# Optimization experiments

Measured on AMD Instinct MI355X. Metric: run time of the kernel, lower is better.

The kernel has to match this reference:

```python
import jax, jax.numpy as jnp
import numpy as np
from jax.ops import segment_sum, segment_max

N = 50000          # nodes
E = 1_600_000      # edges (before self-loops)
IN = 16            # in_channels
F = 20             # N_features
H1 = 4             # heads in conv1
EDGE_DIM = 7
OUT = 3            # out_channels
NEG_SLOPE = 0.2


def setup_inputs() -> dict:
    key = jax.random.key(0)
    ks = jax.random.split(key, 24)
    g = lambda k, shape, fan: (jax.random.normal(k, shape, jnp.float32)
                               * (1.0 / np.sqrt(fan)))
    inp = {}
    inp["x"] = jax.random.normal(ks[0], (N, IN), jnp.float32)
    inp["edge_index"] = jax.random.randint(ks[1], (2, E), 0, N, jnp.int32)
    inp["edge_attr"] = jax.random.normal(ks[2], (E, EDGE_DIM), jnp.float32)
    # conv1: IN -> F, heads=H1, edge_dim=EDGE_DIM
    inp["W1"] = g(ks[3], (IN, H1 * F), IN)
    inp["att_src1"] = g(ks[4], (H1, F), F)
    inp["att_dst1"] = g(ks[5], (H1, F), F)
    inp["We1"] = g(ks[6], (EDGE_DIM, H1 * F), EDGE_DIM)
    inp["att_e1"] = g(ks[7], (H1, F), F)
    inp["b1"] = jnp.zeros((H1 * F,), jnp.float32)
    # conv2: (H1*F) -> F, heads=1, edge_dim=EDGE_DIM
    inp["W2"] = g(ks[8], (H1 * F, F), H1 * F)
    inp["att_src2"] = g(ks[9], (1, F), F)
    inp["att_dst2"] = g(ks[10], (1, F), F)
    inp["We2"] = g(ks[11], (EDGE_DIM, F), EDGE_DIM)
    inp["att_e2"] = g(ks[12], (1, F), F)
    inp["b2"] = jnp.zeros((F,), jnp.float32)
    # decoder: F -> 10 -> OUT
    inp["D1w"] = g(ks[13], (F, 10), F)
    inp["D1b"] = jnp.zeros((10,), jnp.float32)
    inp["D2w"] = g(ks[14], (10, OUT), 10)
    inp["D2b"] = jnp.zeros((OUT,), jnp.float32)
    return inp


def _gat_layer(x, src, dst, eattr, W, a_s, a_d, We, a_e, b, heads, fdim):
    """PyG GATConv (shared src/dst lin, add_self_loops already applied)."""
    n = x.shape[0]
    xh = (x @ W).reshape(n, heads, fdim)                  # [N,H,F]
    eh = (eattr @ We).reshape(-1, heads, fdim)            # [Ea,H,F]
    a_src = jnp.sum(xh * a_s, axis=-1)                    # [N,H]
    a_dst = jnp.sum(xh * a_d, axis=-1)                    # [N,H]
    a_edge = jnp.sum(eh * a_e, axis=-1)                   # [Ea,H]
    logits = a_src[src] + a_dst[dst] + a_edge             # [Ea,H]
    logits = jnp.where(logits >= 0, logits, NEG_SLOPE * logits)
    # segment softmax over destination node
    m = segment_max(logits, dst, num_segments=n)          # [N,H]
    ex = jnp.exp(logits - m[dst])
    denom = segment_sum(ex, dst, num_segments=n)          # [N,H]
    alpha = ex / (denom[dst] + 1e-16)                     # [Ea,H]
    msg = xh[src] * alpha[:, :, None]                     # [Ea,H,F]
    out = segment_sum(msg, dst, num_segments=n)           # [N,H,F]
    return out.reshape(n, heads * fdim) + b


def reference(x, edge_index, edge_attr, W1, att_src1, att_dst1, We1, att_e1,
              b1, W2, att_src2, att_dst2, We2, att_e2, b2, D1w, D1b, D2w, D2b):
    src, dst = edge_index[0], edge_index[1]
    # add self-loops with edge_attr fill_value='mean' (scatter-mean by dst)
    deg = segment_sum(jnp.ones((E,), jnp.float32), dst, num_segments=N)
    mean_attr = segment_sum(edge_attr, dst, num_segments=N) \
        / jnp.maximum(deg, 1.0)[:, None]
    loops = jnp.arange(N, dtype=src.dtype)
    src_a = jnp.concatenate([src, loops])
    dst_a = jnp.concatenate([dst, loops])
    eattr_a = jnp.concatenate([edge_attr, mean_attr], axis=0)
    # conv1 (heads=4, concat) -> elu  (dropouts are no-ops in eval)
    h = _gat_layer(x, src_a, dst_a, eattr_a, W1, att_src1, att_dst1,
                   We1, att_e1, b1, H1, F)
    h = jax.nn.elu(h)
    # conv2 (heads=1) -> elu
    h = _gat_layer(h, src_a, dst_a, eattr_a, W2, att_src2, att_dst2,
                   We2, att_e2, b2, 1, F)
    h = jax.nn.elu(h)
    # decoder MLP
    h = jax.nn.relu(h @ D1w + D1b)
    return h @ D2w + D2b
```

## Files before the change

kernel.cpp:

```cpp
#include <hip/hip_runtime.h>
#include <hip/hip_fp16.h>

constexpr int NN  = 50000;
constexpr int EEg = 1600000;
constexpr int IND = 16;
constexpr int FD  = 20;
constexpr int H1D = 4;
constexpr int ED  = 7;
constexpr int OUTD = 3;
constexpr int FP  = 24;

__device__ __forceinline__ float lrelu(float x) { return x >= 0.0f ? x : 0.2f * x; }
__device__ __forceinline__ float elu(float x)   { return x > 0.0f ? x : expm1f(x); }
__device__ __forceinline__ unsigned pack2(float a, float b) {
    __half2 h = __floats2half2_rn(a, b);
    return *(unsigned*)&h;
}
__device__ __forceinline__ float2 up2(unsigned w) {
    __half2 h = *(__half2*)&w;
    return __half22float2(h);
}

__global__ void k_deg(const int* __restrict__ ei, int* __restrict__ deg,
                      int* __restrict__ rank) {
    int e = blockIdx.x * blockDim.x + threadIdx.x;
    if (e >= EEg) return;
    rank[e] = atomicAdd(&deg[ei[EEg + e]], 1);
}

__global__ void k_ve(const float* __restrict__ We1, const float* __restrict__ ae1,
                     const float* __restrict__ We2, const float* __restrict__ ae2,
                     float* __restrict__ ve1, float* __restrict__ ve2) {
    int t = threadIdx.x;
    if (t < ED * H1D) {
        int d = t >> 2, h = t & 3;
        float s = 0.0f;
        for (int f = 0; f < FD; ++f) s += We1[d * (H1D * FD) + h * FD + f] * ae1[h * FD + f];
        ve1[t] = s;
    } else if (t < ED * H1D + ED) {
        int d = t - ED * H1D;
        float s = 0.0f;
        for (int f = 0; f < FD; ++f) s += We2[d * FD + f] * ae2[f];
        ve2[d] = s;
    }
}

__global__ void k_scanA(const int* __restrict__ deg, int* __restrict__ partial,
                        int* __restrict__ bsum) {
    __shared__ int sd[256];
    int t = threadIdx.x, i = blockIdx.x * 256 + t;
    int v = (i < NN) ? deg[i] : 0;
    sd[t] = v;
    __syncthreads();
    for (int off = 1; off < 256; off <<= 1) {
        int u = (t >= off) ? sd[t - off] : 0;
        __syncthreads();
        sd[t] += u;
        __syncthreads();
    }
    if (i < NN) partial[i] = sd[t] - v;
    if (t == 255) bsum[blockIdx.x] = sd[255];
}
__global__ void k_scanB(const int* __restrict__ bsum, int* __restrict__ boff, int nb) {
    __shared__ int sd[256];
    int t = threadIdx.x;
    int v = (t < nb) ? bsum[t] : 0;
    sd[t] = v;
    __syncthreads();
    for (int off = 1; off < 256; off <<= 1) {
        int u = (t >= off) ? sd[t - off] : 0;
        __syncthreads();
        sd[t] += u;
        __syncthreads();
    }
    if (t < nb) boff[t] = sd[t] - v;
}
__global__ void k_scanC(const int* __restrict__ partial, const int* __restrict__ boff,
                        int* __restrict__ row_off) {
    int i = blockIdx.x * 256 + threadIdx.x;
    if (i < NN) row_off[i] = partial[i] + boff[blockIdx.x];
    if (i == 0) row_off[NN] = EEg;
}

__global__ __launch_bounds__(256) void k_scatter(
        const int* __restrict__ ei, const float* __restrict__ eattr,
        const float* __restrict__ ve1, const float* __restrict__ ve2,
        const int* __restrict__ row_off, const int* __restrict__ rank,
        uint4* __restrict__ csr) {
    __shared__ float sv1[ED * H1D], sv2[ED];
    __shared__ float se[256 * ED];
    if (threadIdx.x < ED * H1D) sv1[threadIdx.x] = ve1[threadIdx.x];
    if (threadIdx.x < ED) sv2[threadIdx.x] = ve2[threadIdx.x];
    size_t gbase = (size_t)blockIdx.x * 256 * ED;
    for (int i = threadIdx.x; i < 256 * ED; i += 256) {
        size_t g = gbase + i;
        if (g < (size_t)EEg * ED) se[i] = eattr[g];
    }
    __syncthreads();
    int e = blockIdx.x * 256 + threadIdx.x;
    if (e >= EEg) return;
    int src = ei[e], dst = ei[EEg + e];
    const float* a = &se[threadIdx.x * ED];
    float v0 = 0.f, v1 = 0.f, v2 = 0.f, v3 = 0.f, w2 = 0.f;
#pragma unroll
    for (int d = 0; d < ED; ++d) {
        float ad = a[d];
        v0 += ad * sv1[d * H1D + 0];
        v1 += ad * sv1[d * H1D + 1];
        v2 += ad * sv1[d * H1D + 2];
        v3 += ad * sv1[d * H1D + 3];
        w2 += ad * sv2[d];
    }
    int slot = row_off[dst] + rank[e];
    uint4 rec;
    rec.x = (unsigned)src;
    rec.y = pack2(v0, v1);
    rec.z = pack2(v2, v3);
    rec.w = pack2(w2, 0.0f);
    csr[slot] = rec;
}

__global__ void k_mean_self(const int* __restrict__ row_off, const uint4* __restrict__ csr,
                            float* __restrict__ a_e1s, float* __restrict__ a_e2s) {
    int n = blockIdx.x * blockDim.x + threadIdx.x;
    if (n >= NN) return;
    int beg = row_off[n], end = row_off[n + 1];
    float s0 = 0.f, s1 = 0.f, s2 = 0.f, s3 = 0.f, se = 0.f;
    for (int j = beg; j < end; ++j) {
        uint4 r = csr[j];
        float2 a01 = up2(r.y), a23 = up2(r.z), ap = up2(r.w);
        s0 += a01.x; s1 += a01.y; s2 += a23.x; s3 += a23.y; se += ap.x;
    }
    float inv = 1.0f / fmaxf((float)(end - beg), 1.0f);
    a_e1s[n * H1D + 0] = s0 * inv;
    a_e1s[n * H1D + 1] = s1 * inv;
    a_e1s[n * H1D + 2] = s2 * inv;
    a_e1s[n * H1D + 3] = s3 * inv;
    a_e2s[n] = se * inv;
}

__global__ void k_xh1attn1(const float* __restrict__ x, const float* __restrict__ W1,
                           const float* __restrict__ as, const float* __restrict__ ad,
                           __half* __restrict__ xh1h, float* __restrict__ a_src1,
                           float* __restrict__ a_dst1) {
    __shared__ float sW[IND * H1D * FD];
    for (int i = threadIdx.x; i < IND * H1D * FD; i += blockDim.x) sW[i] = W1[i];
    __syncthreads();
    int idx = blockIdx.x * blockDim.x + threadIdx.x;
    if (idx >= NN * H1D) return;
    int n = idx >> 2, h = idx & 3;
    float xr[IND];
    const float4* xp = (const float4*)&x[(size_t)n * IND];
#pragma unroll
    for (int q = 0; q < IND / 4; ++q) {
        float4 v = xp[q];
        xr[4 * q] = v.x; xr[4 * q + 1] = v.y; xr[4 * q + 2] = v.z; xr[4 * q + 3] = v.w;
    }
    float ss = 0.f, sd = 0.f;
    float o[FD];
#pragma unroll
    for (int f = 0; f < FD; ++f) {
        float s = 0.f;
#pragma unroll
        for (int k = 0; k < IND; ++k) s += xr[k] * sW[k * (H1D * FD) + h * FD + f];
        o[f] = s;
        ss += s * as[h * FD + f];
        sd += s * ad[h * FD + f];
    }
    uint4* xo = (uint4*)&xh1h[((size_t)n * H1D + h) * FP];
    xo[0] = make_uint4(pack2(o[0], o[1]), pack2(o[2], o[3]), pack2(o[4], o[5]), pack2(o[6], o[7]));
    xo[1] = make_uint4(pack2(o[8], o[9]), pack2(o[10], o[11]), pack2(o[12], o[13]), pack2(o[14], o[15]));
    xo[2] = make_uint4(pack2(o[16], o[17]), pack2(o[18], o[19]), 0u, 0u);
    a_src1[idx] = ss; a_dst1[idx] = sd;
}

#define FMA_PAYLOAD(ex, g0, g1, g2)                                     \
    {                                                                   \
        float2 f_;                                                      \
        f_ = up2(g0.x); acc[0] += (ex) * f_.x;  acc[1] += (ex) * f_.y;  \
        f_ = up2(g0.y); acc[2] += (ex) * f_.x;  acc[3] += (ex) * f_.y;  \
        f_ = up2(g0.z); acc[4] += (ex) * f_.x;  acc[5] += (ex) * f_.y;  \
        f_ = up2(g0.w); acc[6] += (ex) * f_.x;  acc[7] += (ex) * f_.y;  \
        f_ = up2(g1.x); acc[8] += (ex) * f_.x;  acc[9] += (ex) * f_.y;  \
        f_ = up2(g1.y); acc[10] += (ex) * f_.x; acc[11] += (ex) * f_.y; \
        f_ = up2(g1.z); acc[12] += (ex) * f_.x; acc[13] += (ex) * f_.y; \
        f_ = up2(g1.w); acc[14] += (ex) * f_.x; acc[15] += (ex) * f_.y; \
        f_ = up2(g2.x); acc[16] += (ex) * f_.x; acc[17] += (ex) * f_.y; \
        f_ = up2(g2.y); acc[18] += (ex) * f_.x; acc[19] += (ex) * f_.y; \
    }

__global__ __launch_bounds__(256) void k_conv1(
        const int* __restrict__ row_off, const uint4* __restrict__ csr,
        const float* __restrict__ a_src1, const float* __restrict__ a_dst1,
        const float* __restrict__ a_e1s, const __half* __restrict__ xh1h,
        const float* __restrict__ b1, float* __restrict__ h1) {
    int idx = blockIdx.x * 256 + threadIdx.x;
    int n = idx >> 4, low = idx & 15, h = low & 3, p = low >> 2;
    int beg = row_off[n], end = row_off[n + 1];
    float adst = a_dst1[n * H1D + h];
    float m, denom;
    float acc[FD];
#pragma unroll
    for (int f = 0; f < FD; ++f) acc[f] = 0.f;
    if (p == 0) {
        m = lrelu(a_src1[n * H1D + h] + adst + a_e1s[n * H1D + h]);
        denom = 1.0f;
        const uint4* xp = (const uint4*)&xh1h[((size_t)n * H1D + h) * FP];
        uint4 s0 = xp[0], s1 = xp[1];
        uint2 s2 = *(const uint2*)(xp + 2);
        FMA_PAYLOAD(1.0f, s0, s1, s2);
    } else {
        m = -1e30f; denom = 0.f;
    }
    int j = beg + p;
    uint4 rC, gC0, gC1; uint2 gC2; float avC;
    uint4 rN;
    if (j < end) {
        rC = csr[j];
        int s = (int)rC.x;
        avC = a_src1[s * H1D + h];
        const uint4* xp = (const uint4*)&xh1h[((size_t)s * H1D + h) * FP];
        gC0 = xp[0]; gC1 = xp[1]; gC2 = *(const uint2*)(xp + 2);
    }
    if (j + 4 < end) rN = csr[j + 4];
    while (j < end) {
        uint4 rNN;
        if (j + 8 < end) rNN = csr[j + 8];
        float avP; uint4 gP0, gP1; uint2 gP2;
        if (j + 4 < end) {
            int s = (int)rN.x;
            avP = a_src1[s * H1D + h];
            const uint4* xp = (const uint4*)&xh1h[((size_t)s * H1D + h) * FP];
            gP0 = xp[0]; gP1 = xp[1]; gP2 = *(const uint2*)(xp + 2);
        }
        unsigned wae = (h < 2) ? rC.y : rC.z;
        float2 aep = up2(wae);
        float ae = (h & 1) ? aep.y : aep.x;
        float l = lrelu(avC + adst + ae);
        if (l > m) {
            float sc = __expf(m - l);
            denom *= sc;
#pragma unroll
            for (int f = 0; f < FD; ++f) acc[f] *= sc;
            m = l;
        }
        float ex = __expf(l - m);
        denom += ex;
        FMA_PAYLOAD(ex, gC0, gC1, gC2);
        rC = rN; avC = avP; gC0 = gP0; gC1 = gP1; gC2 = gP2;
        rN = rNN;
        j += 4;
    }
#pragma unroll
    for (int st = 4; st <= 8; st <<= 1) {
        float mo = __shfl_xor(m, st);
        float dno = __shfl_xor(denom, st);
        float M = fmaxf(m, mo);
        float ssf = __expf(m - M), sof = __expf(mo - M);
        denom = denom * ssf + dno * sof;
#pragma unroll
        for (int f = 0; f < FD; ++f) acc[f] = acc[f] * ssf + __shfl_xor(acc[f], st) * sof;
        m = M;
    }
    if (p) return;
    float inv = 1.0f / (denom + 1e-16f);
    float* ho = &h1[((size_t)n * H1D + h) * FD];
#pragma unroll
    for (int f = 0; f < FD; ++f) ho[f] = elu(acc[f] * inv + b1[h * FD + f]);
}

__global__ void k_xh2attn2(const float* __restrict__ h1, const float* __restrict__ W2,
                           const float* __restrict__ as, const float* __restrict__ ad,
                           __half* __restrict__ xh2h, float* __restrict__ a_src2,
                           float* __restrict__ a_dst2) {
    __shared__ float sW[H1D * FD * FD];
    for (int i = threadIdx.x; i < H1D * FD * FD; i += blockDim.x) sW[i] = W2[i];
    __syncthreads();
    int n = blockIdx.x * blockDim.x + threadIdx.x;
    if (n >= NN) return;
    float hr[H1D * FD];
    const float4* hp = (const float4*)&h1[(size_t)n * (H1D * FD)];
#pragma unroll
    for (int q = 0; q < (H1D * FD) / 4; ++q) {
        float4 v = hp[q];
        hr[4 * q] = v.x; hr[4 * q + 1] = v.y; hr[4 * q + 2] = v.z; hr[4 * q + 3] = v.w;
    }
    float ss = 0.f, sd = 0.f;
    float o[FD];
#pragma unroll
    for (int f = 0; f < FD; ++f) {
        float s = 0.f;
#pragma unroll
        for (int k = 0; k < H1D * FD; ++k) s += hr[k] * sW[k * FD + f];
        o[f] = s;
        ss += s * as[f];
        sd += s * ad[f];
    }
    uint4* xo = (uint4*)&xh2h[(size_t)n * FP];
    xo[0] = make_uint4(pack2(o[0], o[1]), pack2(o[2], o[3]), pack2(o[4], o[5]), pack2(o[6], o[7]));
    xo[1] = make_uint4(pack2(o[8], o[9]), pack2(o[10], o[11]), pack2(o[12], o[13]), pack2(o[14], o[15]));
    xo[2] = make_uint4(pack2(o[16], o[17]), pack2(o[18], o[19]), 0u, 0u);
    a_src2[n] = ss; a_dst2[n] = sd;
}

__global__ __launch_bounds__(256) void k_conv2dec(
        const int* __restrict__ row_off, const uint4* __restrict__ csr,
        const float* __restrict__ a_src2, const float* __restrict__ a_dst2,
        const float* __restrict__ a_e2s, const __half* __restrict__ xh2h,
        const float* __restrict__ b2, const float* __restrict__ D1w,
        const float* __restrict__ D1b, const float* __restrict__ D2w,
        const float* __restrict__ D2b, float* __restrict__ out) {
    __shared__ float sD1w[FD * 10], sD1b[10], sD2w[10 * OUTD], sD2b[OUTD], sb2[FD];
    for (int i = threadIdx.x; i < FD * 10; i += blockDim.x) sD1w[i] = D1w[i];
    if (threadIdx.x < 10) sD1b[threadIdx.x] = D1b[threadIdx.x];
    if (threadIdx.x < 10 * OUTD) sD2w[threadIdx.x] = D2w[threadIdx.x];
    if (threadIdx.x < OUTD) sD2b[threadIdx.x] = D2b[threadIdx.x];
    if (threadIdx.x < FD) sb2[threadIdx.x] = b2[threadIdx.x];
    __syncthreads();
    int idx = blockIdx.x * 256 + threadIdx.x;
    if (idx >= NN * 4) return;
    int n = idx >> 2, p = idx & 3;
    int beg = row_off[n], end = row_off[n + 1];
    float adst = a_dst2[n];
    float m, denom;
    float acc[FD];
#pragma unroll
    for (int f = 0; f < FD; ++f) acc[f] = 0.f;
    if (p == 0) {
        m = lrelu(a_src2[n] + adst + a_e2s[n]);
        denom = 1.0f;
        const uint4* xp = (const uint4*)&xh2h[(size_t)n * FP];
        uint4 s0 = xp[0], s1 = xp[1];
        uint2 s2 = *(const uint2*)(xp + 2);
        FMA_PAYLOAD(1.0f, s0, s1, s2);
    } else {
        m = -1e30f; denom = 0.f;
    }
    int j = beg + p;
    uint4 rC, gC0, gC1; uint2 gC2; float avC;
    uint4 rN;
    if (j < end) {
        rC = csr[j];
        int s = (int)rC.x;
        avC = a_src2[s];
        const uint4* xp = (const uint4*)&xh2h[(size_t)s * FP];
        gC0 = xp[0]; gC1 = xp[1]; gC2 = *(const uint2*)(xp + 2);
    }
    if (j + 4 < end) rN = csr[j + 4];
    while (j < end) {
        uint4 rNN;
        if (j + 8 < end) rNN = csr[j + 8];
        float avP; uint4 gP0, gP1; uint2 gP2;
        if (j + 4 < end) {
            int s = (int)rN.x;
            avP = a_src2[s];
            const uint4* xp = (const uint4*)&xh2h[(size_t)s * FP];
            gP0 = xp[0]; gP1 = xp[1]; gP2 = *(const uint2*)(xp + 2);
        }
        float l = lrelu(avC + adst + up2(rC.w).x);
        if (l > m) {
            float sc = __expf(m - l);
            denom *= sc;
#pragma unroll
            for (int f = 0; f < FD; ++f) acc[f] *= sc;
            m = l;
        }
        float ex = __expf(l - m);
        denom += ex;
        FMA_PAYLOAD(ex, gC0, gC1, gC2);
        rC = rN; avC = avP; gC0 = gP0; gC1 = gP1; gC2 = gP2;
        rN = rNN;
        j += 4;
    }
#pragma unroll
    for (int st = 1; st <= 2; st <<= 1) {
        float mo = __shfl_xor(m, st);
        float dno = __shfl_xor(denom, st);
        float M = fmaxf(m, mo);
        float ssf = __expf(m - M), sof = __expf(mo - M);
        denom = denom * ssf + dno * sof;
#pragma unroll
        for (int f = 0; f < FD; ++f) acc[f] = acc[f] * ssf + __shfl_xor(acc[f], st) * sof;
        m = M;
    }
    if (p) return;
    float inv = 1.0f / (denom + 1e-16f);
    float h2[FD];
#pragma unroll
    for (int f = 0; f < FD; ++f) h2[f] = elu(acc[f] * inv + sb2[f]);
    float o[OUTD];
#pragma unroll
    for (int k = 0; k < OUTD; ++k) o[k] = sD2b[k];
    for (int j2 = 0; j2 < 10; ++j2) {
        float hid = sD1b[j2];
#pragma unroll
        for (int f = 0; f < FD; ++f) hid += h2[f] * sD1w[f * 10 + j2];
        hid = fmaxf(hid, 0.0f);
#pragma unroll
        for (int k = 0; k < OUTD; ++k) o[k] += hid * sD2w[j2 * OUTD + k];
    }
#pragma unroll
    for (int k = 0; k < OUTD; ++k) out[n * OUTD + k] = o[k];
}

extern "C" void kernel_launch(void* const* d_in, const int* in_sizes, int n_in,
                              void* d_out, int out_size, void* d_ws, size_t ws_size,
                              hipStream_t stream) {
    const float* x     = (const float*)d_in[0];
    const int*   ei    = (const int*)d_in[1];
    const float* eattr = (const float*)d_in[2];
    const float* W1    = (const float*)d_in[3];
    const float* as1   = (const float*)d_in[4];
    const float* ad1   = (const float*)d_in[5];
    const float* We1   = (const float*)d_in[6];
    const float* ae1   = (const float*)d_in[7];
    const float* b1    = (const float*)d_in[8];
    const float* W2    = (const float*)d_in[9];
    const float* as2   = (const float*)d_in[10];
    const float* ad2   = (const float*)d_in[11];
    const float* We2   = (const float*)d_in[12];
    const float* ae2   = (const float*)d_in[13];
    const float* b2    = (const float*)d_in[14];
    const float* D1w   = (const float*)d_in[15];
    const float* D1b   = (const float*)d_in[16];
    const float* D2w   = (const float*)d_in[17];
    const float* D2b   = (const float*)d_in[18];
    float* out = (float*)d_out;

    float* w = (float*)d_ws;
    size_t o = 0;
    int*   deg = (int*)(w + o); o += NN;
    size_t zero_bytes = o * sizeof(float);
    int*   rank    = (int*)(w + o); o += EEg;
    int*   partial = (int*)(w + o); o += NN;
    int*   bsum    = (int*)(w + o); o += 256;
    int*   boff    = (int*)(w + o); o += 256;
    int*   row_off = (int*)(w + o); o += NN + 4;
    float* csr     = w + o; o += (size_t)EEg * 4;
    float* ve1     = w + o; o += 32;
    float* ve2     = w + o; o += 8;
    float* a_e1s   = w + o; o += (size_t)NN * H1D;
    float* a_e2s   = w + o; o += NN;
    float* a_src1  = w + o; o += (size_t)NN * H1D;
    float* a_dst1  = w + o; o += (size_t)NN * H1D;
    __half* xh1h   = (__half*)(w + o); o += (size_t)NN * H1D * FP / 2;
    float* h1      = w + o; o += (size_t)NN * H1D * FD;
    __half* xh2h   = (__half*)(w + o); o += (size_t)NN * FP / 2;
    float* a_src2  = w + o; o += NN;
    float* a_dst2  = w + o; o += NN;

    hipMemsetAsync(d_ws, 0, zero_bytes, stream);

    const int B = 256;
    auto cdiv = [](long a, long b) { return (int)((a + b - 1) / b); };
    const int NB = cdiv(NN, 256);

    k_deg<<<cdiv(EEg, B), B, 0, stream>>>(ei, deg, rank);
    k_ve<<<1, 64, 0, stream>>>(We1, ae1, We2, ae2, ve1, ve2);
    k_scanA<<<NB, 256, 0, stream>>>(deg, partial, bsum);
    k_scanB<<<1, 256, 0, stream>>>(bsum, boff, NB);
    k_scanC<<<NB, 256, 0, stream>>>(partial, boff, row_off);
    k_scatter<<<cdiv(EEg, B), B, 0, stream>>>(ei, eattr, ve1, ve2, row_off, rank,
                                              (uint4*)csr);
    k_mean_self<<<NB, 256, 0, stream>>>(row_off, (const uint4*)csr, a_e1s, a_e2s);
    k_xh1attn1<<<cdiv((long)NN * H1D, B), B, 0, stream>>>(x, W1, as1, ad1, xh1h, a_src1,
                                                          a_dst1);
    k_conv1<<<cdiv((long)NN * 16, 256), 256, 0, stream>>>(row_off, (const uint4*)csr,
                                                          a_src1, a_dst1, a_e1s, xh1h, b1,
                                                          h1);
    k_xh2attn2<<<NB, 256, 0, stream>>>(h1, W2, as2, ad2, xh2h, a_src2, a_dst2);
    k_conv2dec<<<cdiv((long)NN * 4, 256), 256, 0, stream>>>(row_off, (const uint4*)csr,
                                                            a_src2, a_dst2, a_e2s, xh2h,
                                                            b2, D1w, D1b, D2w, D2b, out);
}
```

Baseline: 280.2 us.

## Replace atomic-rank CSR build with two-pass LSD radix bucketing by destination

Builds the destination-sorted edge list with a two-pass radix partition instead of a global atomic degree count plus scan. The first pass histograms the low 8 bits of dst per block and scatters packed records to a temporary buffer using shared-memory atomics. The second pass buckets each bin by the high bits to produce the final CSR with per-node begin and degree arrays. This removes the contended global atomics, the rank array and the memset. In exchange it adds an extra full pass over the edge records, packs dst into the upper 16 bits of a record word (which fits only because N is at most 65535), and the first kernel launches only 256 blocks.

```diff
diff --git a/kernel.cpp b/kernel.cpp
--- a/kernel.cpp
+++ b/kernel.cpp
@@ -9,6 +9,9 @@
 constexpr int ED  = 7;
 constexpr int OUTD = 3;
 constexpr int FP  = 24;
+constexpr int NB2 = 256;
+constexpr int EPB = EEg / NB2;
+constexpr int NH  = 196;
 
 __device__ __forceinline__ float lrelu(float x) { return x >= 0.0f ? x : 0.2f * x; }
 __device__ __forceinline__ float elu(float x)   { return x > 0.0f ? x : expm1f(x); }
@@ -19,13 +22,6 @@
 __device__ __forceinline__ float2 up2(unsigned w) {
     __half2 h = *(__half2*)&w;
     return __half22float2(h);
-}
-
-__global__ void k_deg(const int* __restrict__ ei, int* __restrict__ deg,
-                      int* __restrict__ rank) {
-    int e = blockIdx.x * blockDim.x + threadIdx.x;
-    if (e >= EEg) return;
-    rank[e] = atomicAdd(&deg[ei[EEg + e]], 1);
 }
 
 __global__ void k_ve(const float* __restrict__ We1, const float* __restrict__ ae1,
@@ -45,86 +41,132 @@
     }
 }
 
-__global__ void k_scanA(const int* __restrict__ deg, int* __restrict__ partial,
-                        int* __restrict__ bsum) {
+__global__ __launch_bounds__(256) void k_h1(const int* __restrict__ ei,
+                                            int* __restrict__ bh1T) {
+    __shared__ int lh[256];
+    lh[threadIdx.x] = 0;
+    __syncthreads();
+    int base0 = blockIdx.x * EPB;
+    for (int off = 0; off < EPB; off += 256) {
+        int i = off + threadIdx.x;
+        if (i < EPB) atomicAdd(&lh[ei[EEg + base0 + i] & 255], 1);
+    }
+    __syncthreads();
+    bh1T[threadIdx.x * NB2 + blockIdx.x] = lh[threadIdx.x];
+}
+
+__global__ void k_colscan(const int* __restrict__ bh1T, int* __restrict__ off1,
+                          int* __restrict__ binStart) {
+    int tid = threadIdx.x;
+    int total = 0;
+#pragma unroll 8
+    for (int b = 0; b < NB2; ++b) total += bh1T[tid * NB2 + b];
     __shared__ int sd[256];
-    int t = threadIdx.x, i = blockIdx.x * 256 + t;
-    int v = (i < NN) ? deg[i] : 0;
-    sd[t] = v;
+    sd[tid] = total;
     __syncthreads();
     for (int off = 1; off < 256; off <<= 1) {
-        int u = (t >= off) ? sd[t - off] : 0;
+        int u = (tid >= off) ? sd[tid - off] : 0;
         __syncthreads();
-        sd[t] += u;
+        sd[tid] += u;
         __syncthreads();
     }
-    if (i < NN) partial[i] = sd[t] - v;
-    if (t == 255) bsum[blockIdx.x] = sd[255];
-}
-__global__ void k_scanB(const int* __restrict__ bsum, int* __restrict__ boff, int nb) {
-    __shared__ int sd[256];
-    int t = threadIdx.x;
-    int v = (t < nb) ? bsum[t] : 0;
-    sd[t] = v;
-    __syncthreads();
-    for (int off = 1; off < 256; off <<= 1) {
-        int u = (t >= off) ? sd[t - off] : 0;
-        __syncthreads();
-        sd[t] += u;
-        __syncthreads();
-    }
-    if (t < nb) boff[t] = sd[t] - v;
-}
-__global__ void k_scanC(const int* __restrict__ partial, const int* __restrict__ boff,
-                        int* __restrict__ row_off) {
-    int i = blockIdx.x * 256 + threadIdx.x;
-    if (i < NN) row_off[i] = partial[i] + boff[blockIdx.x];
-    if (i == 0) row_off[NN] = EEg;
-}
-
-__global__ __launch_bounds__(256) void k_scatter(
+    int excl = sd[tid] - total;
+    binStart[tid] = excl;
+    if (tid == 255) binStart[256] = excl + total;
+    int run = excl;
+#pragma unroll 8
+    for (int b = 0; b < NB2; ++b) {
+        off1[b * 256 + tid] = run;
+        run += bh1T[tid * NB2 + b];
+    }
+}
+
+__global__ __launch_bounds__(256) void k_sc1(
         const int* __restrict__ ei, const float* __restrict__ eattr,
         const float* __restrict__ ve1, const float* __restrict__ ve2,
-        const int* __restrict__ row_off, const int* __restrict__ rank,
-        uint4* __restrict__ csr) {
+        const int* __restrict__ off1, uint4* __restrict__ tmp) {
     __shared__ float sv1[ED * H1D], sv2[ED];
     __shared__ float se[256 * ED];
+    __shared__ int cur[256];
     if (threadIdx.x < ED * H1D) sv1[threadIdx.x] = ve1[threadIdx.x];
     if (threadIdx.x < ED) sv2[threadIdx.x] = ve2[threadIdx.x];
-    size_t gbase = (size_t)blockIdx.x * 256 * ED;
-    for (int i = threadIdx.x; i < 256 * ED; i += 256) {
-        size_t g = gbase + i;
-        if (g < (size_t)EEg * ED) se[i] = eattr[g];
-    }
-    __syncthreads();
-    int e = blockIdx.x * 256 + threadIdx.x;
-    if (e >= EEg) return;
-    int src = ei[e], dst = ei[EEg + e];
-    const float* a = &se[threadIdx.x * ED];
-    float v0 = 0.f, v1 = 0.f, v2 = 0.f, v3 = 0.f, w2 = 0.f;
-#pragma unroll
-    for (int d = 0; d < ED; ++d) {
-        float ad = a[d];
-        v0 += ad * sv1[d * H1D + 0];
-        v1 += ad * sv1[d * H1D + 1];
-        v2 += ad * sv1[d * H1D + 2];
-        v3 += ad * sv1[d * H1D + 3];
-        w2 += ad * sv2[d];
-    }
-    int slot = row_off[dst] + rank[e];
-    uint4 rec;
-    rec.x = (unsigned)src;
-    rec.y = pack2(v0, v1);
-    rec.z = pack2(v2, v3);
-    rec.w = pack2(w2, 0.0f);
-    csr[slot] = rec;
-}
-
-__global__ void k_mean_self(const int* __restrict__ row_off, const uint4* __restrict__ csr,
+    cur[threadIdx.x] = off1[blockIdx.x * 256 + threadIdx.x];
+    int base0 = blockIdx.x * EPB;
+    for (int off = 0; off < EPB; off += 256) {
+        int cnt = min(256, EPB - off);
+        __syncthreads();
+        for (int i = threadIdx.x; i < cnt * ED; i += 256)
+            se[i] = eattr[(size_t)(base0 + off) * ED + i];
+        __syncthreads();
+        if (threadIdx.x < cnt) {
+            int e = base0 + off + threadIdx.x;
+            int src = ei[e], dst = ei[EEg + e];
+            const float* a = &se[threadIdx.x * ED];
+            float v0 = 0.f, v1 = 0.f, v2 = 0.f, v3 = 0.f, w2 = 0.f;
+#pragma unroll
+            for (int d = 0; d < ED; ++d) {
+                float ad = a[d];
+                v0 += ad * sv1[d * H1D + 0];
+                v1 += ad * sv1[d * H1D + 1];
+                v2 += ad * sv1[d * H1D + 2];
+                v3 += ad * sv1[d * H1D + 3];
+                w2 += ad * sv2[d];
+            }
+            int pos = atomicAdd(&cur[dst & 255], 1);
+            uint4 rec;
+            rec.x = (unsigned)src;
+            rec.y = pack2(v0, v1);
+            rec.z = pack2(v2, v3);
+            rec.w = (pack2(w2, 0.0f) & 0xFFFFu) | ((unsigned)dst << 16);
+            tmp[pos] = rec;
+        }
+    }
+}
+
+__global__ __launch_bounds__(256) void k_bucket(
+        const int* __restrict__ binStart, const uint4* __restrict__ tmp,
+        uint4* __restrict__ csr, int* __restrict__ begA, int* __restrict__ degA) {
+    int L = blockIdx.x, tid = threadIdx.x;
+    int s = binStart[L], t = binStart[L + 1];
+    __shared__ int lh[NH];
+    __shared__ int sd[256];
+    __shared__ int cur[NH];
+    for (int i = tid; i < NH; i += 256) lh[i] = 0;
+    __syncthreads();
+    for (int j = s + tid; j < t; j += 256) {
+        unsigned dst = tmp[j].w >> 16;
+        atomicAdd(&lh[dst >> 8], 1);
+    }
+    __syncthreads();
+    int v = (tid < NH) ? lh[tid] : 0;
+    sd[tid] = v;
+    __syncthreads();
+    for (int off = 1; off < 256; off <<= 1) {
+        int u = (tid >= off) ? sd[tid - off] : 0;
+        __syncthreads();
+        sd[tid] += u;
+        __syncthreads();
+    }
+    int excl = sd[tid] - v;
+    if (tid < NH) {
+        int d = (tid << 8) | L;
+        if (d < NN) { begA[d] = s + excl; degA[d] = v; }
+        cur[tid] = s + excl;
+    }
+    __syncthreads();
+    for (int j = s + tid; j < t; j += 256) {
+        uint4 r = tmp[j];
+        int pos = atomicAdd(&cur[(r.w >> 16) >> 8], 1);
+        csr[pos] = r;
+    }
+}
+
+__global__ void k_mean_self(const int* __restrict__ begA, const int* __restrict__ degA,
+                            const uint4* __restrict__ csr,
                             float* __restrict__ a_e1s, float* __restrict__ a_e2s) {
     int n = blockIdx.x * blockDim.x + threadIdx.x;
     if (n >= NN) return;
-    int beg = row_off[n], end = row_off[n + 1];
+    int beg = begA[n], end = beg + degA[n];
     float s0 = 0.f, s1 = 0.f, s2 = 0.f, s3 = 0.f, se = 0.f;
     for (int j = beg; j < end; ++j) {
         uint4 r = csr[j];
@@ -190,13 +232,14 @@
     }
 
 __global__ __launch_bounds__(256) void k_conv1(
-        const int* __restrict__ row_off, const uint4* __restrict__ csr,
+        const int* __restrict__ begA, const int* __restrict__ degA,
+        const uint4* __restrict__ csr,
         const float* __restrict__ a_src1, const float* __restrict__ a_dst1,
         const float* __restrict__ a_e1s, const __half* __restrict__ xh1h,
         const float* __restrict__ b1, float* __restrict__ h1) {
     int idx = blockIdx.x * 256 + threadIdx.x;
     int n = idx >> 4, low = idx & 15, h = low & 3, p = low >> 2;
-    int beg = row_off[n], end = row_off[n + 1];
+    int beg = begA[n], end = beg + degA[n];
     float adst = a_dst1[n * H1D + h];
     float m, denom;
     float acc[FD];
@@ -304,7 +347,8 @@
 }
 
 __global__ __launch_bounds__(256) void k_conv2dec(
-        const int* __restrict__ row_off, const uint4* __restrict__ csr,
+        const int* __restrict__ begA, const int* __restrict__ degA,
+        const uint4* __restrict__ csr,
         const float* __restrict__ a_src2, const float* __restrict__ a_dst2,
         const float* __restrict__ a_e2s, const __half* __restrict__ xh2h,
         const float* __restrict__ b2, const float* __restrict__ D1w,
@@ -320,7 +364,7 @@
     int idx = blockIdx.x * 256 + threadIdx.x;
     if (idx >= NN * 4) return;
     int n = idx >> 2, p = idx & 3;
-    int beg = row_off[n], end = row_off[n + 1];
+    int beg = begA[n], end = beg + degA[n];
     float adst = a_dst2[n];
     float m, denom;
     float acc[FD];
@@ -429,13 +473,12 @@
 
     float* w = (float*)d_ws;
     size_t o = 0;
-    int*   deg = (int*)(w + o); o += NN;
-    size_t zero_bytes = o * sizeof(float);
-    int*   rank    = (int*)(w + o); o += EEg;
-    int*   partial = (int*)(w + o); o += NN;
-    int*   bsum    = (int*)(w + o); o += 256;
-    int*   boff    = (int*)(w + o); o += 256;
-    int*   row_off = (int*)(w + o); o += NN + 4;
+    int*   bh1T    = (int*)(w + o); o += (size_t)256 * NB2;
+    int*   off1    = (int*)(w + o); o += (size_t)NB2 * 256;
+    int*   binStart= (int*)(w + o); o += 260;
+    int*   begA    = (int*)(w + o); o += NN;
+    int*   degA    = (int*)(w + o); o += NN;
+    float* tmp     = w + o; o += (size_t)EEg * 4;
     float* csr     = w + o; o += (size_t)EEg * 4;
     float* ve1     = w + o; o += 32;
     float* ve2     = w + o; o += 8;
@@ -449,27 +492,24 @@
     float* a_src2  = w + o; o += NN;
     float* a_dst2  = w + o; o += NN;
 
-    hipMemsetAsync(d_ws, 0, zero_bytes, stream);
-
     const int B = 256;
     auto cdiv = [](long a, long b) { return (int)((a + b - 1) / b); };
     const int NB = cdiv(NN, 256);
 
-    k_deg<<<cdiv(EEg, B), B, 0, stream>>>(ei, deg, rank);
     k_ve<<<1, 64, 0, stream>>>(We1, ae1, We2, ae2, ve1, ve2);
-    k_scanA<<<NB, 256, 0, stream>>>(deg, partial, bsum);
-    k_scanB<<<1, 256, 0, stream>>>(bsum, boff, NB);
-    k_scanC<<<NB, 256, 0, stream>>>(partial, boff, row_off);
-    k_scatter<<<cdiv(EEg, B), B, 0, stream>>>(ei, eattr, ve1, ve2, row_off, rank,
-                                              (uint4*)csr);
-    k_mean_self<<<NB, 256, 0, stream>>>(row_off, (const uint4*)csr, a_e1s, a_e2s);
+    k_h1<<<NB2, 256, 0, stream>>>(ei, bh1T);
+    k_colscan<<<1, 256, 0, stream>>>(bh1T, off1, binStart);
+    k_sc1<<<NB2, 256, 0, stream>>>(ei, eattr, ve1, ve2, off1, (uint4*)tmp);
+    k_bucket<<<256, 256, 0, stream>>>(binStart, (const uint4*)tmp, (uint4*)csr, begA,
+                                      degA);
+    k_mean_self<<<NB, 256, 0, stream>>>(begA, degA, (const uint4*)csr, a_e1s, a_e2s);
     k_xh1attn1<<<cdiv((long)NN * H1D, B), B, 0, stream>>>(x, W1, as1, ad1, xh1h, a_src1,
                                                           a_dst1);
-    k_conv1<<<cdiv((long)NN * 16, 256), 256, 0, stream>>>(row_off, (const uint4*)csr,
+    k_conv1<<<cdiv((long)NN * 16, 256), 256, 0, stream>>>(begA, degA, (const uint4*)csr,
                                                           a_src1, a_dst1, a_e1s, xh1h, b1,
                                                           h1);
     k_xh2attn2<<<NB, 256, 0, stream>>>(h1, W2, as2, ad2, xh2h, a_src2, a_dst2);
-    k_conv2dec<<<cdiv((long)NN * 4, 256), 256, 0, stream>>>(row_off, (const uint4*)csr,
+    k_conv2dec<<<cdiv((long)NN * 4, 256), 256, 0, stream>>>(begA, degA, (const uint4*)csr,
                                                             a_src2, a_dst2, a_e2s, xh2h,
                                                             b2, D1w, D1b, D2w, D2b, out);
 }
```

Measured after the change: 283.7 us. No clear change (+1.3%).
